# Kernel tuning notes

Hardware: AMD Instinct MI355X
Metric: run time of the kernel (lower is better)

## Reference

```python
import jax, jax.numpy as jnp
import numpy as np
from jax import lax

EPS = 1e-5

def _bn(x, p):
    # p: [4, C] = (gamma, beta, running_mean, running_var); x: [B,C,H,W] (eval-mode BN)
    g, b, m, v = p
    return (x - m[None, :, None, None]) * (g / jnp.sqrt(v + EPS))[None, :, None, None] + b[None, :, None, None]

def _relu6(x):
    return jnp.clip(x, 0.0, 6.0)

def _grouped_1x1(x, w):
    # x: [B, D, H, W], w: [G, D//G]; groups=G, 1 out channel per group (contiguous channel groups)
    B, D, H, W = x.shape
    G = w.shape[0]
    xr = x.reshape(B, G, D // G, H, W)
    return jnp.einsum('bgihw,gi->bghw', xr, w)

def _pool4(x, kind):
    if kind == 'max':
        return lax.reduce_window(x, -jnp.inf, lax.max, (1, 1, 4, 4), (1, 1, 4, 4), 'VALID')
    s = lax.reduce_window(x, 0.0, lax.add, (1, 1, 4, 4), (1, 1, 4, 4), 'VALID')
    return s / 16.0

def _rel_pos_index(rh):
    # Swin-style relative position index, static numpy
    coords = np.stack(np.meshgrid(np.arange(rh), np.arange(rh), indexing='ij')).reshape(2, -1)
    rel = coords[:, :, None] - coords[:, None, :]
    rel = rel.transpose(1, 2, 0).astype(np.int64)
    rel[..., 0] += rh - 1
    rel[..., 1] += rh - 1
    rel[..., 0] *= 2 * rh - 1
    return rel.sum(-1)  # [N, N]

def _upsample_bilinear_align(x, scale):
    # UpsamplingBilinear2d => align_corners=True
    B, C, H, W = x.shape
    Ho, Wo = H * scale, W * scale
    ys = jnp.linspace(0.0, H - 1.0, Ho)
    xs = jnp.linspace(0.0, W - 1.0, Wo)
    y0 = jnp.floor(ys).astype(jnp.int32); y1 = jnp.minimum(y0 + 1, H - 1); wy = (ys - y0)[None, None, :, None]
    x0 = jnp.floor(xs).astype(jnp.int32); x1 = jnp.minimum(x0 + 1, W - 1); wx = (xs - x0)[None, None, None, :]
    rows = x[:, :, y0, :] * (1.0 - wy) + x[:, :, y1, :] * wy          # [B,C,Ho,W]
    return rows[:, :, :, x0] * (1.0 - wx) + rows[:, :, :, x1] * wx    # [B,C,Ho,Wo]

def bh_attention(x, w_le, b_le, bn_le, w_max, b_max, bn_max, w_avg, b_avg, bn_avg,
                 bias_table, w_q, w_kv, w_proj, b_proj, w_out, b_out):
    D = x.shape[1]
    G = D // 4
    # q branch: 4x4 stride-4 grouped conv (groups=G, 4 in-ch per group) + BN + ReLU6
    xq = lax.conv_general_dilated(x, w_le, window_strides=(4, 4), padding='VALID',
                                  dimension_numbers=('NCHW', 'OIHW', 'NCHW'),
                                  feature_group_count=G)
    xq = _relu6(_bn(xq + b_le[None, :, None, None], bn_le))
    B, C, H, W = xq.shape
    N = H * W
    nH = 4 if C > 64 else 2
    hd = C // nH
    xq_t = xq.reshape(B, C, N).transpose(0, 2, 1)                      # [B,N,C]
    q = (xq_t @ w_q).reshape(B, N, nH, hd).transpose(0, 2, 1, 3) * (hd ** -0.5)

    def kv_branch(t, w_g, b_g, bn_g):
        t = _relu6(_bn(_grouped_1x1(t, w_g) + b_g[None, :, None, None], bn_g))
        tt = t.reshape(B, C, N).transpose(0, 2, 1)                     # [B,N,C]
        kv = (tt @ w_kv).reshape(B, N, 2, nH, hd).transpose(2, 0, 3, 1, 4)
        return kv[0], kv[1]                                            # [B,nH,N,hd]

    k1, v1 = kv_branch(_pool4(x, 'max'), w_max, b_max, bn_max)
    k2, v2 = kv_branch(_pool4(x, 'avg'), w_avg, b_avg, bn_avg)

    idx = _rel_pos_index(H)
    bias = bias_table[idx.reshape(-1)].reshape(N, N, nH).transpose(2, 0, 1)[None]  # [1,nH,N,N]

    def attend(k, v):
        attn = jax.nn.softmax(jnp.einsum('bhnd,bhmd->bhnm', q, k) + bias, axis=-1)
        o = jnp.einsum('bhnm,bhmd->bhnd', attn, v).transpose(0, 2, 1, 3).reshape(B, N, C)
        return o @ w_proj + b_proj

    x1 = attend(k1, v1).reshape(B, H, W, C).transpose(0, 3, 1, 2)
    x2 = attend(k2, v2).reshape(B, H, W, C).transpose(0, 3, 1, 2)
    out = x1 + x2
    out = jnp.einsum('bchw,oc->bohw', out, w_out) + b_out[None, :, None, None]
    return _upsample_bilinear_align(out, 4)


def setup_inputs() -> dict:
    key = jax.random.key(0)
    dim, h, B = 384, 128, 8
    C = dim // 4            # 96
    nH = 4 if C > 64 else 2
    rh = h // 4             # 32
    ks = jax.random.split(key, 12)
    bn_id = jnp.stack([jnp.ones(C), jnp.zeros(C), jnp.zeros(C), jnp.ones(C)])
    inp = {
        'x': jax.random.normal(ks[0], (B, dim, h, h), jnp.float32),
        'w_le': jax.random.normal(ks[1], (C, 4, 4, 4), jnp.float32) * 0.05,
        'b_le': jnp.zeros((C,), jnp.float32),
        'bn_le': bn_id,
        'w_max': jax.random.normal(ks[2], (C, 4), jnp.float32) * 0.1,
        'b_max': jnp.zeros((C,), jnp.float32),
        'bn_max': bn_id,
        'w_avg': jax.random.normal(ks[3], (C, 4), jnp.float32) * 0.1,
        'b_avg': jnp.zeros((C,), jnp.float32),
        'bn_avg': bn_id,
        'bias_table': jax.random.normal(ks[4], ((2 * rh - 1) ** 2, nH), jnp.float32) * 0.02,
        'w_q': jax.random.normal(ks[5], (C, C), jnp.float32) * (C ** -0.5),
        'w_kv': jax.random.normal(ks[6], (C, 2 * C), jnp.float32) * (C ** -0.5),
        'w_proj': jax.random.normal(ks[7], (C, C), jnp.float32) * (C ** -0.5),
        'b_proj': jnp.zeros((C,), jnp.float32),
        'w_out': jax.random.normal(ks[8], (dim, C), jnp.float32) * (C ** -0.5),
        'b_out': jnp.zeros((dim,), jnp.float32),
    }
    return inp


def reference(x, w_le, b_le, bn_le, w_max, b_max, bn_max, w_avg, b_avg, bn_avg,
              bias_table, w_q, w_kv, w_proj, b_proj, w_out, b_out):
    return bh_attention(x, w_le, b_le, bn_le, w_max, b_max, bn_max, w_avg, b_avg, bn_avg,
                        bias_table, w_q, w_kv, w_proj, b_proj, w_out, b_out)
```

## Files before the change

### kernel.cpp

```cpp
#include <hip/hip_runtime.h>
#include <math.h>

namespace {
constexpr int Bb  = 8;
constexpr int Dd  = 384;
constexpr int HIN = 128;
constexpr int Cc  = 96;
constexpr int Nn  = 1024;
constexpr int NH  = 4;
constexpr int HD  = 24;
}
#define BN_EPS 1e-5f
#define QSCALE 0.20412414523193154f

typedef unsigned short u16;
typedef unsigned int   u32;
typedef __attribute__((ext_vector_type(8))) short bh8;
typedef __attribute__((ext_vector_type(4))) float fx4;

#define MFMA16(a,b,c) __builtin_amdgcn_mfma_f32_16x16x32_bf16((a),(b),(c),0,0,0)

union PackU { u32 u[4]; bh8 s; };

__device__ __forceinline__ void split1(float v, u16& hi, u16& lo) {
    const u32 bv = __float_as_uint(v);
    const u32 hb = bv & 0xffff0000u;
    hi = (u16)(bv >> 16);
    const float r = v - __uint_as_float(hb);
    lo = (u16)(__float_as_uint(r) >> 16);
}
__device__ __forceinline__ void split2(float x, float y, u32& hi, u32& lo) {
    const u32 bx = __float_as_uint(x), by = __float_as_uint(y);
    const u32 hx = bx & 0xffff0000u, hy = by & 0xffff0000u;
    hi = (hx >> 16) | hy;
    const float rx = x - __uint_as_float(hx);
    const float ry = y - __uint_as_float(hy);
    lo = (__float_as_uint(rx) >> 16) | (__float_as_uint(ry) & 0xffff0000u);
}

__device__ __forceinline__ float bn_relu6(float y, const float* __restrict__ bn, int c) {
    float gam = bn[c], bet = bn[Cc + c], mu = bn[2*Cc + c], var = bn[3*Cc + c];
    float s = gam / sqrtf(var + BN_EPS);
    float r = (y - mu) * s + bet;
    return fminf(fmaxf(r, 0.0f), 6.0f);
}

__global__ __launch_bounds__(256) void stem_kernel(
    const float* __restrict__ x, const float* __restrict__ w_le,
    const float* __restrict__ b_le, const float* __restrict__ bn_le,
    const float* __restrict__ w_max, const float* __restrict__ b_max, const float* __restrict__ bn_max,
    const float* __restrict__ w_avg, const float* __restrict__ b_avg, const float* __restrict__ bn_avg,
    const float* __restrict__ w_proj, const float* __restrict__ b_proj,
    const float* __restrict__ w_out, const float* __restrict__ b_out,
    const float* __restrict__ btab,
    float* __restrict__ xq, float* __restrict__ tmx, float* __restrict__ tav,
    float* __restrict__ wf, float* __restrict__ bf, float* __restrict__ btr)
{
    const int tid = threadIdx.x;
    if (blockIdx.y == 96) {
        const int tg = (blockIdx.z*4 + blockIdx.x)*256 + tid;
        for (int e = tg; e < Cc*Dd; e += 8192) {
            const int c = e / Dd, o = e - c*Dd;
            const float* wp = w_proj + c*Cc;
            const float* wo = w_out + (size_t)o*Cc;
            float acc = 0.0f;
            for (int c2 = 0; c2 < Cc; ++c2) acc = fmaf(wp[c2], wo[c2], acc);
            wf[e] = acc;
        }
        if (tg < Dd) {
            const float* wo = w_out + (size_t)tg*Cc;
            float acc = 0.0f;
            for (int c = 0; c < Cc; ++c) acc = fmaf(b_proj[c], wo[c], acc);
            bf[tg] = b_out[tg] + 2.0f * acc;
        }
        for (int e = tg; e < 3969*NH; e += 8192) {
            const int hh = e / 3969, i = e - hh*3969;
            btr[e] = btab[i*NH + hh];
        }
        return;
    }
    const int n = blockIdx.x * 256 + tid;
    const int g = blockIdx.y;
    const int b = blockIdx.z;
    const int oh = n >> 5, ow = n & 31;

    const float* xb = x + (((size_t)b * Dd + 4*g) * HIN + 4*oh) * HIN + 4*ow;
    float conv = 0.0f, mxv = 0.0f, avv = 0.0f;
    #pragma unroll
    for (int i = 0; i < 4; ++i) {
        float cmax = -3.0e38f, csum = 0.0f;
        #pragma unroll
        for (int kh = 0; kh < 4; ++kh) {
            const float4 v = *(const float4*)(xb + ((size_t)i * HIN + kh) * HIN);
            const float* wl = w_le + (((g*4 + i)*4 + kh) * 4);
            conv = fmaf(v.x, wl[0], conv);
            conv = fmaf(v.y, wl[1], conv);
            conv = fmaf(v.z, wl[2], conv);
            conv = fmaf(v.w, wl[3], conv);
            cmax = fmaxf(cmax, fmaxf(fmaxf(v.x, v.y), fmaxf(v.z, v.w)));
            csum += (v.x + v.y) + (v.z + v.w);
        }
        mxv = fmaf(cmax, w_max[g*4 + i], mxv);
        avv = fmaf(csum * (1.0f/16.0f), w_avg[g*4 + i], avv);
    }
    const float xqv = bn_relu6(conv + b_le[g], bn_le, g);
    const float tm  = bn_relu6(mxv  + b_max[g], bn_max, g);
    const float ta  = bn_relu6(avv  + b_avg[g], bn_avg, g);
    const size_t o = ((size_t)b * Cc + g) * Nn + n;
    xq[o] = xqv; tmx[o] = tm; tav[o] = ta;
}

__global__ __launch_bounds__(256, 3) void proj_kernel(
    const float* __restrict__ xq, const float* __restrict__ tmx, const float* __restrict__ tav,
    const float* __restrict__ w_q, const float* __restrict__ w_kv,
    u16* __restrict__ qhp, u16* __restrict__ qlp,
    u16* __restrict__ k1h, u16* __restrict__ k1l, u16* __restrict__ k2h, u16* __restrict__ k2l,
    u16* __restrict__ v1h, u16* __restrict__ v1l, u16* __restrict__ v2h, u16* __restrict__ v2l)
{
    const int tid   = threadIdx.x;
    const int n0    = blockIdx.x * 32;
    const int b     = blockIdx.y;
    const int phase = blockIdx.z;
    __shared__ float A[32*97];
    __shared__ float lw[96*96];

    const float* asrc = (phase == 0) ? xq : ((phase == 1 || phase == 3) ? tmx : tav);
    for (int e = tid; e < 96*32; e += 256) {
        const int c = e >> 5, j = e & 31;
        A[j*97 + c] = asrc[((size_t)b * Cc + c) * Nn + n0 + j];
    }
    const float* wsrc = (phase == 0) ? w_q : w_kv;
    const int RS = (phase == 0) ? 96 : 192;
    const int WO = (phase <= 2) ? 0 : 96;
    for (int e = tid; e < 96*96; e += 256)
        lw[e] = wsrc[(e/96)*RS + WO + (e%96)];
    __syncthreads();

    const int tn = (tid & 7) * 4;
    const int tc = (tid >> 3) * 3;

    float acc[4][3] = {};
    for (int k = 0; k < 96; ++k) {
        const float w0 = lw[k*96 + tc + 0];
        const float w1 = lw[k*96 + tc + 1];
        const float w2 = lw[k*96 + tc + 2];
        #pragma unroll
        for (int i = 0; i < 4; ++i) {
            const float a = A[(tn+i)*97 + k];
            acc[i][0] = fmaf(a, w0, acc[i][0]);
            acc[i][1] = fmaf(a, w1, acc[i][1]);
            acc[i][2] = fmaf(a, w2, acc[i][2]);
        }
    }

    u16* dh; u16* dl;
    if      (phase == 0) { dh = qhp; dl = qlp; }
    else if (phase == 1) { dh = k1h; dl = k1l; }
    else if (phase == 2) { dh = k2h; dl = k2l; }
    else if (phase == 3) { dh = v1h; dl = v1l; }
    else                 { dh = v2h; dl = v2l; }

    #pragma unroll
    for (int j = 0; j < 3; ++j) {
        const int col = tc + j, hh = col / HD, d = col - hh*HD;
        #pragma unroll
        for (int i = 0; i < 4; ++i) {
            const int n = n0 + tn + i;
            float v = acc[i][j];
            size_t dst;
            if (phase == 0) {
                v *= QSCALE;
                dst = ((size_t)(b*NH + hh)*Nn + n)*32 + d;
            } else if (phase <= 2) {
                const int rho = (n & ~31) | ((n & 4) << 2) | ((n & 24) >> 1) | (n & 3);
                dst = ((size_t)(b*NH + hh)*Nn + rho)*32 + d;
            } else {
                dst = ((size_t)(b*NH + hh)*32 + d)*Nn + n;
            }
            u16 hi, lo;
            split1(v, hi, lo);
            dh[dst] = hi; dl[dst] = lo;
        }
    }

    for (int e = tid; e < 1024; e += 256) {
        const int hh = e >> 8;
        const int nn = (e >> 3) & 31;
        const int d  = 24 + (e & 7);
        const int n  = n0 + nn;
        const size_t dst = (phase <= 2)
            ? ((size_t)(b*NH + hh)*Nn + n)*32 + d
            : ((size_t)(b*NH + hh)*32 + d)*Nn + n;
        dh[dst] = 0; dl[dst] = 0;
    }
}

__global__ __launch_bounds__(256, 4) void attn_kernel(
    const u16* __restrict__ qhp, const u16* __restrict__ qlp,
    const u16* __restrict__ k1h, const u16* __restrict__ k1l,
    const u16* __restrict__ k2h, const u16* __restrict__ k2l,
    const u16* __restrict__ v1h, const u16* __restrict__ v1l,
    const u16* __restrict__ v2h, const u16* __restrict__ v2l,
    const float* __restrict__ btr, float* __restrict__ osum)
{
    const int tid = threadIdx.x;
    const int h = blockIdx.y, b = blockIdx.z;
    const int bh = b*NH + h;

    __shared__ float biasl[3969];
    __shared__ float mrg[2][64][21];

    for (int e = tid; e < 3969; e += 256) biasl[e] = btr[h*3969 + e];
    __syncthreads();

    const int lane = tid & 63;
    const int wave = tid >> 6;
    const int qg = wave & 1;
    const int ks = wave >> 1;
    const int lg = lane >> 4;
    const int lr = lane & 15;
    const int q  = blockIdx.x*32 + qg*16 + lr;
    const int yn = q >> 5, xn = q & 31;

    const size_t qoff = ((size_t)bh*Nn + q)*32 + lg*8;
    const bh8 qfh = *(const bh8*)(qhp + qoff);
    const bh8 qfl = *(const bh8*)(qlp + qoff);

    const size_t kbase = ((size_t)bh*Nn + lr)*32 + lg*8;
    const size_t vbase = ((size_t)bh*32 + lr)*Nn + lg*8;
    const u16* kph[2] = { k1h + kbase, k2h + kbase };
    const u16* kpl[2] = { k1l + kbase, k2l + kbase };
    const u16* vph[2] = { v1h + vbase, v2h + vbase };
    const u16* vpl[2] = { v1l + vbase, v2l + vbase };

    const fx4 zero = {0.0f, 0.0f, 0.0f, 0.0f};
    fx4 oo[2][2];
    float mm[2], ll[2];

    #pragma unroll
    for (int br = 0; br < 2; ++br) {
        oo[br][0] = zero; oo[br][1] = zero;
        float m = -3.0e38f, l = 0.0f;
        const u16* kh = kph[br]; const u16* kl = kpl[br];
        const u16* vh = vph[br]; const u16* vl = vpl[br];

        for (int it = ks*8; it < ks*8 + 8; ++it) {
            const int kb = it*64;
            fx4 s[4];
            #pragma unroll
            for (int t = 0; t < 4; ++t) {
                const int ro = (kb + t*16)*32;
                const bh8 ah = *(const bh8*)(kh + ro);
                const bh8 al = *(const bh8*)(kl + ro);
                const int ym   = (kb >> 5) + (t >> 1);
                const int xmb  = (t & 1)*4 + lg*8;
                const int rowb = (yn - ym + 31)*63 + (xn + 31) - xmb;
                fx4 u;
                #pragma unroll
                for (int j = 0; j < 4; ++j) u[j] = biasl[rowb - j];
                u = MFMA16(ah, qfh, u);
                u = MFMA16(ah, qfl, u);
                u = MFMA16(al, qfh, u);
                s[t] = u;
            }

            float lmax = fmaxf(fmaxf(s[0][0], s[0][1]), fmaxf(s[0][2], s[0][3]));
            #pragma unroll
            for (int t = 1; t < 4; ++t)
                lmax = fmaxf(lmax, fmaxf(fmaxf(s[t][0], s[t][1]), fmaxf(s[t][2], s[t][3])));

            if (!__all(lmax <= m + 8.0f)) {
                float tmax = lmax;
                tmax = fmaxf(tmax, __shfl_xor(tmax, 16));
                tmax = fmaxf(tmax, __shfl_xor(tmax, 32));
                const float M = fmaxf(m, tmax);
                const float c = __expf(m - M);
                l *= c;
                oo[br][0] *= c; oo[br][1] *= c;
                m = M;
            }

            #pragma unroll
            for (int ch = 0; ch < 2; ++ch) {
                const float e0 = __expf(s[2*ch  ][0] - m);
                const float e1 = __expf(s[2*ch  ][1] - m);
                const float e2 = __expf(s[2*ch  ][2] - m);
                const float e3 = __expf(s[2*ch  ][3] - m);
                const float e4 = __expf(s[2*ch+1][0] - m);
                const float e5 = __expf(s[2*ch+1][1] - m);
                const float e6 = __expf(s[2*ch+1][2] - m);
                const float e7 = __expf(s[2*ch+1][3] - m);
                l += ((e0 + e1) + (e2 + e3)) + ((e4 + e5) + (e6 + e7));
                PackU ph_, pl_;
                split2(e0, e1, ph_.u[0], pl_.u[0]);
                split2(e2, e3, ph_.u[1], pl_.u[1]);
                split2(e4, e5, ph_.u[2], pl_.u[2]);
                split2(e6, e7, ph_.u[3], pl_.u[3]);
                const int vo0 = kb + ch*32;
                #pragma unroll
                for (int dt = 0; dt < 2; ++dt) {
                    const size_t vo = (size_t)(dt*16)*Nn + vo0;
                    const bh8 wh = *(const bh8*)(vh + vo);
                    const bh8 wl = *(const bh8*)(vl + vo);
                    oo[br][dt] = MFMA16(wh, ph_.s, oo[br][dt]);
                    oo[br][dt] = MFMA16(wh, pl_.s, oo[br][dt]);
                    oo[br][dt] = MFMA16(wl, ph_.s, oo[br][dt]);
                }
            }
        }
        mm[br] = m; ll[br] = l;
    }

    if (ks == 1) {
        float* mb = &mrg[qg][lane][0];
        #pragma unroll
        for (int br = 0; br < 2; ++br) {
            mb[br*10 + 0] = mm[br];
            mb[br*10 + 1] = ll[br];
            #pragma unroll
            for (int j = 0; j < 4; ++j) {
                mb[br*10 + 2 + j] = oo[br][0][j];
                mb[br*10 + 6 + j] = oo[br][1][j];
            }
        }
    }
    __syncthreads();
    if (ks == 0) {
        const float* mb = &mrg[qg][lane][0];
        float li[2]; fx4 om[2][2];
        #pragma unroll
        for (int br = 0; br < 2; ++br) {
            const float mo  = mb[br*10 + 0];
            const float lo2 = mb[br*10 + 1];
            const float M  = fmaxf(mm[br], mo);
            const float ca = __expf(mm[br] - M);
            const float cb = __expf(mo - M);
            float lm = ll[br]*ca + lo2*cb;
            #pragma unroll
            for (int dt = 0; dt < 2; ++dt)
                #pragma unroll
                for (int j = 0; j < 4; ++j)
                    om[br][dt][j] = oo[br][dt][j]*ca + mb[br*10 + 2 + dt*4 + j]*cb;
            lm += __shfl_xor(lm, 16);
            lm += __shfl_xor(lm, 32);
            li[br] = 1.0f / lm;
        }
        float* orow = osum + ((size_t)b*Nn + q)*Cc + h*HD;
        #pragma unroll
        for (int dt = 0; dt < 2; ++dt)
            #pragma unroll
            for (int j = 0; j < 4; ++j) {
                const int d = dt*16 + lg*4 + j;
                if (d < HD) orow[d] = om[0][dt][j]*li[0] + om[1][dt][j]*li[1];
            }
    }
}

__global__ __launch_bounds__(256) void outgemm_kernel(
    const float* __restrict__ osum, const float* __restrict__ wf, const float* __restrict__ bf,
    float* __restrict__ outs)
{
    const int tid = threadIdx.x;
    const int n0 = blockIdx.x * 32;
    const int b  = blockIdx.y;
    const int o0 = blockIdx.z * 128;
    __shared__ float ax[32*97];
    __shared__ float lw[96*128];
    for (int e = tid; e < 32*96; e += 256) {
        const int n = e / 96, c = e - n*96;
        ax[n*97 + c] = osum[((size_t)b*Nn + n0 + n)*Cc + c];
    }
    for (int e = tid; e < 96*128; e += 256) {
        const int c = e >> 7, j = e & 127;
        lw[c*128 + j] = wf[(size_t)c*Dd + o0 + j];
    }
    __syncthreads();
    const int tn = (tid & 7) * 4;
    const int tj = (tid >> 3) * 4;
    float acc[4][4] = {};
    for (int c = 0; c < 96; ++c) {
        const float4 wv = *(const float4*)&lw[c*128 + tj];
        #pragma unroll
        for (int i = 0; i < 4; ++i) {
            const float a = ax[(tn+i)*97 + c];
            acc[i][0] = fmaf(a, wv.x, acc[i][0]);
            acc[i][1] = fmaf(a, wv.y, acc[i][1]);
            acc[i][2] = fmaf(a, wv.z, acc[i][2]);
            acc[i][3] = fmaf(a, wv.w, acc[i][3]);
        }
    }
    #pragma unroll
    for (int j = 0; j < 4; ++j) {
        const int o = o0 + tj + j;
        const float bb = bf[o];
        #pragma unroll
        for (int i = 0; i < 4; ++i)
            outs[((size_t)b*Dd + o)*Nn + n0 + tn + i] = acc[i][j] + bb;
    }
}

__global__ __launch_bounds__(256) void upsample_kernel(
    const float* __restrict__ src, float* __restrict__ dst)
{
    const int gid = blockIdx.x * 256 + threadIdx.x;
    const int ox4 = gid & 31;
    const int oy  = (gid >> 5) & 127;
    const int bc  = gid >> 12;
    const float* s = src + (size_t)bc * 1024;
    const float sy = oy * (31.0f / 127.0f);
    const int y0 = (int)sy;
    const int y1 = min(y0 + 1, 31);
    const float wy = sy - (float)y0;
    const float* r0 = s + y0 * 32;
    const float* r1 = s + y1 * 32;
    float res[4];
    #pragma unroll
    for (int j = 0; j < 4; ++j) {
        const int ox = ox4 * 4 + j;
        const float sx = ox * (31.0f / 127.0f);
        const int x0 = (int)sx;
        const int x1 = min(x0 + 1, 31);
        const float wx = sx - (float)x0;
        const float t0 = r0[x0] * (1.0f - wx) + r0[x1] * wx;
        const float t1 = r1[x0] * (1.0f - wx) + r1[x1] * wx;
        res[j] = t0 * (1.0f - wy) + t1 * wy;
    }
    *(float4*)(dst + (size_t)gid * 4) = make_float4(res[0], res[1], res[2], res[3]);
}

extern "C" void kernel_launch(void* const* d_in, const int* in_sizes, int n_in,
                              void* d_out, int out_size, void* d_ws, size_t ws_size,
                              hipStream_t stream)
{
    const float* x      = (const float*)d_in[0];
    const float* w_le   = (const float*)d_in[1];
    const float* b_le   = (const float*)d_in[2];
    const float* bn_le  = (const float*)d_in[3];
    const float* w_max  = (const float*)d_in[4];
    const float* b_max  = (const float*)d_in[5];
    const float* bn_max = (const float*)d_in[6];
    const float* w_avg  = (const float*)d_in[7];
    const float* b_avg  = (const float*)d_in[8];
    const float* bn_avg = (const float*)d_in[9];
    const float* btab   = (const float*)d_in[10];
    const float* w_q    = (const float*)d_in[11];
    const float* w_kv   = (const float*)d_in[12];
    const float* w_proj = (const float*)d_in[13];
    const float* b_proj = (const float*)d_in[14];
    const float* w_out  = (const float*)d_in[15];
    const float* b_out  = (const float*)d_in[16];
    (void)in_sizes; (void)n_in; (void)out_size; (void)ws_size;

    float* ws = (float*)d_ws;
    const size_t T  = (size_t)Bb * Cc * Nn;
    const size_t AS = (size_t)Bb * NH * Nn * 32;

    float* xq   = ws + 0*T;
    float* tmx  = ws + 1*T;
    float* tav  = ws + 2*T;
    u16*  bb16  = (u16*)(ws + 3*T);
    u16* qh  = bb16 + 0*AS;  u16* ql  = bb16 + 1*AS;
    u16* k1h = bb16 + 2*AS;  u16* k1l = bb16 + 3*AS;
    u16* k2h = bb16 + 4*AS;  u16* k2l = bb16 + 5*AS;
    u16* v1h = bb16 + 6*AS;  u16* v1l = bb16 + 7*AS;
    u16* v2h = bb16 + 8*AS;  u16* v2l = bb16 + 9*AS;
    float* osum = (float*)(bb16 + 10*AS);
    float* wf   = osum + T;
    float* bf   = wf + (size_t)Cc*Dd;
    float* btr  = bf + Dd;
    float* outs = ws;

    stem_kernel<<<dim3(4, 97, 8), 256, 0, stream>>>(
        x, w_le, b_le, bn_le, w_max, b_max, bn_max, w_avg, b_avg, bn_avg,
        w_proj, b_proj, w_out, b_out, btab, xq, tmx, tav, wf, bf, btr);
    proj_kernel<<<dim3(32, 8, 5), 256, 0, stream>>>(
        xq, tmx, tav, w_q, w_kv, qh, ql, k1h, k1l, k2h, k2l, v1h, v1l, v2h, v2l);
    attn_kernel<<<dim3(32, 4, 8), 256, 0, stream>>>(
        qh, ql, k1h, k1l, k2h, k2l, v1h, v1l, v2h, v2l, btr, osum);
    outgemm_kernel<<<dim3(32, 8, 3), 256, 0, stream>>>(osum, wf, bf, outs);
    upsample_kernel<<<dim3(49152), 256, 0, stream>>>(outs, (float*)d_out);
}
```

Measured before the change: 539.1 us.

## Split attention across branches into single-wave blocks sharing K/V over two query tiles

```diff
diff --git a/kernel.cpp b/kernel.cpp
--- a/kernel.cpp
+++ b/kernel.cpp
@@ -195,169 +195,171 @@
     }
 }
 
-__global__ __launch_bounds__(256, 4) void attn_kernel(
+__global__ __launch_bounds__(64) void attn_kernel(
     const u16* __restrict__ qhp, const u16* __restrict__ qlp,
     const u16* __restrict__ k1h, const u16* __restrict__ k1l,
     const u16* __restrict__ k2h, const u16* __restrict__ k2l,
     const u16* __restrict__ v1h, const u16* __restrict__ v1l,
     const u16* __restrict__ v2h, const u16* __restrict__ v2l,
-    const float* __restrict__ btr, float* __restrict__ osum)
+    const float* __restrict__ btr,
+    float* __restrict__ osum1, float* __restrict__ osum2)
 {
     const int tid = threadIdx.x;
-    const int h = blockIdx.y, b = blockIdx.z;
+    const int h  = blockIdx.y;
+    const int b  = blockIdx.z >> 1;
+    const int br = blockIdx.z & 1;
     const int bh = b*NH + h;
 
     __shared__ float biasl[3969];
-    __shared__ float mrg[2][64][21];
-
-    for (int e = tid; e < 3969; e += 256) biasl[e] = btr[h*3969 + e];
+    for (int e = tid; e < 3969; e += 64) biasl[e] = btr[h*3969 + e];
     __syncthreads();
 
-    const int lane = tid & 63;
-    const int wave = tid >> 6;
-    const int qg = wave & 1;
-    const int ks = wave >> 1;
-    const int lg = lane >> 4;
-    const int lr = lane & 15;
-    const int q  = blockIdx.x*32 + qg*16 + lr;
-    const int yn = q >> 5, xn = q & 31;
-
-    const size_t qoff = ((size_t)bh*Nn + q)*32 + lg*8;
-    const bh8 qfh = *(const bh8*)(qhp + qoff);
-    const bh8 qfl = *(const bh8*)(qlp + qoff);
-
-    const size_t kbase = ((size_t)bh*Nn + lr)*32 + lg*8;
-    const size_t vbase = ((size_t)bh*32 + lr)*Nn + lg*8;
-    const u16* kph[2] = { k1h + kbase, k2h + kbase };
-    const u16* kpl[2] = { k1l + kbase, k2l + kbase };
-    const u16* vph[2] = { v1h + vbase, v2h + vbase };
-    const u16* vpl[2] = { v1l + vbase, v2l + vbase };
+    const int lg = tid >> 4;
+    const int lr = tid & 15;
+    const int q0 = blockIdx.x * 32;
+    const int qA = q0 + lr;
+    const int yn = q0 >> 5;
+
+    const u16* kh = br ? k2h : k1h;
+    const u16* kl = br ? k2l : k1l;
+    const u16* vh = br ? v2h : v1h;
+    const u16* vl = br ? v2l : v1l;
+    float* osb    = br ? osum2 : osum1;
+
+    const size_t qoff = ((size_t)bh*Nn + qA)*32 + lg*8;
+    const bh8 qAh = *(const bh8*)(qhp + qoff);
+    const bh8 qAl = *(const bh8*)(qlp + qoff);
+    const bh8 qBh = *(const bh8*)(qhp + qoff + 512);
+    const bh8 qBl = *(const bh8*)(qlp + qoff + 512);
+
+    kh += ((size_t)bh*Nn + lr)*32 + lg*8;
+    kl += ((size_t)bh*Nn + lr)*32 + lg*8;
+    vh += ((size_t)bh*32 + lr)*Nn + lg*8;
+    vl += ((size_t)bh*32 + lr)*Nn + lg*8;
 
     const fx4 zero = {0.0f, 0.0f, 0.0f, 0.0f};
-    fx4 oo[2][2];
-    float mm[2], ll[2];
-
-    #pragma unroll
-    for (int br = 0; br < 2; ++br) {
-        oo[br][0] = zero; oo[br][1] = zero;
-        float m = -3.0e38f, l = 0.0f;
-        const u16* kh = kph[br]; const u16* kl = kpl[br];
-        const u16* vh = vph[br]; const u16* vl = vpl[br];
-
-        for (int it = ks*8; it < ks*8 + 8; ++it) {
-            const int kb = it*64;
-            fx4 s[4];
-            #pragma unroll
-            for (int t = 0; t < 4; ++t) {
-                const int ro = (kb + t*16)*32;
-                const bh8 ah = *(const bh8*)(kh + ro);
-                const bh8 al = *(const bh8*)(kl + ro);
-                const int ym   = (kb >> 5) + (t >> 1);
-                const int xmb  = (t & 1)*4 + lg*8;
-                const int rowb = (yn - ym + 31)*63 + (xn + 31) - xmb;
-                fx4 u;
-                #pragma unroll
-                for (int j = 0; j < 4; ++j) u[j] = biasl[rowb - j];
-                u = MFMA16(ah, qfh, u);
-                u = MFMA16(ah, qfl, u);
-                u = MFMA16(al, qfh, u);
-                s[t] = u;
-            }
-
-            float lmax = fmaxf(fmaxf(s[0][0], s[0][1]), fmaxf(s[0][2], s[0][3]));
-            #pragma unroll
-            for (int t = 1; t < 4; ++t)
-                lmax = fmaxf(lmax, fmaxf(fmaxf(s[t][0], s[t][1]), fmaxf(s[t][2], s[t][3])));
-
-            if (!__all(lmax <= m + 8.0f)) {
-                float tmax = lmax;
-                tmax = fmaxf(tmax, __shfl_xor(tmax, 16));
-                tmax = fmaxf(tmax, __shfl_xor(tmax, 32));
-                const float M = fmaxf(m, tmax);
-                const float c = __expf(m - M);
-                l *= c;
-                oo[br][0] *= c; oo[br][1] *= c;
-                m = M;
-            }
-
-            #pragma unroll
-            for (int ch = 0; ch < 2; ++ch) {
-                const float e0 = __expf(s[2*ch  ][0] - m);
-                const float e1 = __expf(s[2*ch  ][1] - m);
-                const float e2 = __expf(s[2*ch  ][2] - m);
-                const float e3 = __expf(s[2*ch  ][3] - m);
-                const float e4 = __expf(s[2*ch+1][0] - m);
-                const float e5 = __expf(s[2*ch+1][1] - m);
-                const float e6 = __expf(s[2*ch+1][2] - m);
-                const float e7 = __expf(s[2*ch+1][3] - m);
-                l += ((e0 + e1) + (e2 + e3)) + ((e4 + e5) + (e6 + e7));
-                PackU ph_, pl_;
-                split2(e0, e1, ph_.u[0], pl_.u[0]);
-                split2(e2, e3, ph_.u[1], pl_.u[1]);
-                split2(e4, e5, ph_.u[2], pl_.u[2]);
-                split2(e6, e7, ph_.u[3], pl_.u[3]);
-                const int vo0 = kb + ch*32;
-                #pragma unroll
-                for (int dt = 0; dt < 2; ++dt) {
-                    const size_t vo = (size_t)(dt*16)*Nn + vo0;
-                    const bh8 wh = *(const bh8*)(vh + vo);
-                    const bh8 wl = *(const bh8*)(vl + vo);
-                    oo[br][dt] = MFMA16(wh, ph_.s, oo[br][dt]);
-                    oo[br][dt] = MFMA16(wh, pl_.s, oo[br][dt]);
-                    oo[br][dt] = MFMA16(wl, ph_.s, oo[br][dt]);
-                }
-            }
-        }
-        mm[br] = m; ll[br] = l;
-    }
-
-    if (ks == 1) {
-        float* mb = &mrg[qg][lane][0];
-        #pragma unroll
-        for (int br = 0; br < 2; ++br) {
-            mb[br*10 + 0] = mm[br];
-            mb[br*10 + 1] = ll[br];
+    fx4 oA[2] = {zero, zero}, oB[2] = {zero, zero};
+    float mA = -3.0e38f, mB = -3.0e38f, lA = 0.0f, lB = 0.0f;
+
+    for (int it = 0; it < 16; ++it) {
+        const int kb = it*64;
+        fx4 sA[4], sB[4];
+        #pragma unroll
+        for (int t = 0; t < 4; ++t) {
+            const int ro = (kb + t*16)*32;
+            const bh8 ah = *(const bh8*)(kh + ro);
+            const bh8 al = *(const bh8*)(kl + ro);
+            const int ym   = (kb >> 5) + (t >> 1);
+            const int xmb  = (t & 1)*4 + lg*8;
+            const int rowb = (yn - ym + 31)*63 + (lr + 31) - xmb;
+            fx4 uA, uB;
             #pragma unroll
             for (int j = 0; j < 4; ++j) {
-                mb[br*10 + 2 + j] = oo[br][0][j];
-                mb[br*10 + 6 + j] = oo[br][1][j];
+                uA[j] = biasl[rowb - j];
+                uB[j] = biasl[rowb + 16 - j];
             }
-        }
-    }
-    __syncthreads();
-    if (ks == 0) {
-        const float* mb = &mrg[qg][lane][0];
-        float li[2]; fx4 om[2][2];
-        #pragma unroll
-        for (int br = 0; br < 2; ++br) {
-            const float mo  = mb[br*10 + 0];
-            const float lo2 = mb[br*10 + 1];
-            const float M  = fmaxf(mm[br], mo);
-            const float ca = __expf(mm[br] - M);
-            const float cb = __expf(mo - M);
-            float lm = ll[br]*ca + lo2*cb;
+            uA = MFMA16(ah, qAh, uA);
+            uA = MFMA16(ah, qAl, uA);
+            uA = MFMA16(al, qAh, uA);
+            uB = MFMA16(ah, qBh, uB);
+            uB = MFMA16(ah, qBl, uB);
+            uB = MFMA16(al, qBh, uB);
+            sA[t] = uA; sB[t] = uB;
+        }
+
+        float lmA = fmaxf(fmaxf(sA[0][0], sA[0][1]), fmaxf(sA[0][2], sA[0][3]));
+        float lmB = fmaxf(fmaxf(sB[0][0], sB[0][1]), fmaxf(sB[0][2], sB[0][3]));
+        #pragma unroll
+        for (int t = 1; t < 4; ++t) {
+            lmA = fmaxf(lmA, fmaxf(fmaxf(sA[t][0], sA[t][1]), fmaxf(sA[t][2], sA[t][3])));
+            lmB = fmaxf(lmB, fmaxf(fmaxf(sB[t][0], sB[t][1]), fmaxf(sB[t][2], sB[t][3])));
+        }
+        if (!__all(lmA <= mA + 8.0f)) {
+            float tmax = lmA;
+            tmax = fmaxf(tmax, __shfl_xor(tmax, 16));
+            tmax = fmaxf(tmax, __shfl_xor(tmax, 32));
+            const float M = fmaxf(mA, tmax);
+            const float c = __expf(mA - M);
+            lA *= c; oA[0] *= c; oA[1] *= c;
+            mA = M;
+        }
+        if (!__all(lmB <= mB + 8.0f)) {
+            float tmax = lmB;
+            tmax = fmaxf(tmax, __shfl_xor(tmax, 16));
+            tmax = fmaxf(tmax, __shfl_xor(tmax, 32));
+            const float M = fmaxf(mB, tmax);
+            const float c = __expf(mB - M);
+            lB *= c; oB[0] *= c; oB[1] *= c;
+            mB = M;
+        }
+
+        #pragma unroll
+        for (int ch = 0; ch < 2; ++ch) {
+            const float a0 = __expf(sA[2*ch  ][0] - mA);
+            const float a1 = __expf(sA[2*ch  ][1] - mA);
+            const float a2 = __expf(sA[2*ch  ][2] - mA);
+            const float a3 = __expf(sA[2*ch  ][3] - mA);
+            const float a4 = __expf(sA[2*ch+1][0] - mA);
+            const float a5 = __expf(sA[2*ch+1][1] - mA);
+            const float a6 = __expf(sA[2*ch+1][2] - mA);
+            const float a7 = __expf(sA[2*ch+1][3] - mA);
+            lA += ((a0 + a1) + (a2 + a3)) + ((a4 + a5) + (a6 + a7));
+            const float b0 = __expf(sB[2*ch  ][0] - mB);
+            const float b1 = __expf(sB[2*ch  ][1] - mB);
+            const float b2 = __expf(sB[2*ch  ][2] - mB);
+            const float b3 = __expf(sB[2*ch  ][3] - mB);
+            const float b4 = __expf(sB[2*ch+1][0] - mB);
+            const float b5 = __expf(sB[2*ch+1][1] - mB);
+            const float b6 = __expf(sB[2*ch+1][2] - mB);
+            const float b7 = __expf(sB[2*ch+1][3] - mB);
+            lB += ((b0 + b1) + (b2 + b3)) + ((b4 + b5) + (b6 + b7));
+
+            PackU pAh, pAl, pBh, pBl;
+            split2(a0, a1, pAh.u[0], pAl.u[0]);
+            split2(a2, a3, pAh.u[1], pAl.u[1]);
+            split2(a4, a5, pAh.u[2], pAl.u[2]);
+            split2(a6, a7, pAh.u[3], pAl.u[3]);
+            split2(b0, b1, pBh.u[0], pBl.u[0]);
+            split2(b2, b3, pBh.u[1], pBl.u[1]);
+            split2(b4, b5, pBh.u[2], pBl.u[2]);
+            split2(b6, b7, pBh.u[3], pBl.u[3]);
+
+            const int vo0 = kb + ch*32;
             #pragma unroll
-            for (int dt = 0; dt < 2; ++dt)
-                #pragma unroll
-                for (int j = 0; j < 4; ++j)
-                    om[br][dt][j] = oo[br][dt][j]*ca + mb[br*10 + 2 + dt*4 + j]*cb;
-            lm += __shfl_xor(lm, 16);
-            lm += __shfl_xor(lm, 32);
-            li[br] = 1.0f / lm;
-        }
-        float* orow = osum + ((size_t)b*Nn + q)*Cc + h*HD;
-        #pragma unroll
-        for (int dt = 0; dt < 2; ++dt)
-            #pragma unroll
-            for (int j = 0; j < 4; ++j) {
-                const int d = dt*16 + lg*4 + j;
-                if (d < HD) orow[d] = om[0][dt][j]*li[0] + om[1][dt][j]*li[1];
+            for (int dt = 0; dt < 2; ++dt) {
+                const size_t vo = (size_t)(dt*16)*Nn + vo0;
+                const bh8 wh_ = *(const bh8*)(vh + vo);
+                const bh8 wl_ = *(const bh8*)(vl + vo);
+                oA[dt] = MFMA16(wh_, pAh.s, oA[dt]);
+                oA[dt] = MFMA16(wh_, pAl.s, oA[dt]);
+                oA[dt] = MFMA16(wl_, pAh.s, oA[dt]);
+                oB[dt] = MFMA16(wh_, pBh.s, oB[dt]);
+                oB[dt] = MFMA16(wh_, pBl.s, oB[dt]);
+                oB[dt] = MFMA16(wl_, pBh.s, oB[dt]);
             }
-    }
+        }
+    }
+
+    lA += __shfl_xor(lA, 16); lA += __shfl_xor(lA, 32);
+    lB += __shfl_xor(lB, 16); lB += __shfl_xor(lB, 32);
+    const float iA = 1.0f / lA, iB = 1.0f / lB;
+    float* orowA = osb + ((size_t)b*Nn + qA)*Cc + h*HD;
+    float* orowB = orowA + 16*Cc;
+    #pragma unroll
+    for (int dt = 0; dt < 2; ++dt)
+        #pragma unroll
+        for (int j = 0; j < 4; ++j) {
+            const int d = dt*16 + lg*4 + j;
+            if (d < HD) {
+                orowA[d] = oA[dt][j]*iA;
+                orowB[d] = oB[dt][j]*iB;
+            }
+        }
 }
 
 __global__ __launch_bounds__(256) void outgemm_kernel(
-    const float* __restrict__ osum, const float* __restrict__ wf, const float* __restrict__ bf,
+    const float* __restrict__ osum1, const float* __restrict__ osum2,
+    const float* __restrict__ wf, const float* __restrict__ bf,
     float* __restrict__ outs)
 {
     const int tid = threadIdx.x;
@@ -368,7 +370,8 @@
     __shared__ float lw[96*128];
     for (int e = tid; e < 32*96; e += 256) {
         const int n = e / 96, c = e - n*96;
-        ax[n*97 + c] = osum[((size_t)b*Nn + n0 + n)*Cc + c];
+        const size_t src = ((size_t)b*Nn + n0 + n)*Cc + c;
+        ax[n*97 + c] = osum1[src] + osum2[src];
     }
     for (int e = tid; e < 96*128; e += 256) {
         const int c = e >> 7, j = e & 127;
@@ -464,19 +467,20 @@
     u16* k2h = bb16 + 4*AS;  u16* k2l = bb16 + 5*AS;
     u16* v1h = bb16 + 6*AS;  u16* v1l = bb16 + 7*AS;
     u16* v2h = bb16 + 8*AS;  u16* v2l = bb16 + 9*AS;
-    float* osum = (float*)(bb16 + 10*AS);
-    float* wf   = osum + T;
-    float* bf   = wf + (size_t)Cc*Dd;
-    float* btr  = bf + Dd;
-    float* outs = ws;
+    float* osum1 = (float*)(bb16 + 10*AS);
+    float* wf    = osum1 + T;
+    float* bf    = wf + (size_t)Cc*Dd;
+    float* btr   = bf + Dd;
+    float* osum2 = btr + 4*3969;
+    float* outs  = ws;
 
     stem_kernel<<<dim3(4, 97, 8), 256, 0, stream>>>(
         x, w_le, b_le, bn_le, w_max, b_max, bn_max, w_avg, b_avg, bn_avg,
         w_proj, b_proj, w_out, b_out, btab, xq, tmx, tav, wf, bf, btr);
     proj_kernel<<<dim3(32, 8, 5), 256, 0, stream>>>(
         xq, tmx, tav, w_q, w_kv, qh, ql, k1h, k1l, k2h, k2l, v1h, v1l, v2h, v2l);
-    attn_kernel<<<dim3(32, 4, 8), 256, 0, stream>>>(
-        qh, ql, k1h, k1l, k2h, k2l, v1h, v1l, v2h, v2l, btr, osum);
-    outgemm_kernel<<<dim3(32, 8, 3), 256, 0, stream>>>(osum, wf, bf, outs);
+    attn_kernel<<<dim3(32, 4, 16), 64, 0, stream>>>(
+        qh, ql, k1h, k1l, k2h, k2l, v1h, v1l, v2h, v2l, btr, osum1, osum2);
+    outgemm_kernel<<<dim3(32, 8, 3), 256, 0, stream>>>(osum1, osum2, wf, bf, outs);
     upsample_kernel<<<dim3(49152), 256, 0, stream>>>(outs, (float*)d_out);
 }
```

Measured after the change: 506.1 us. 6.1% less time.
